# Kernel optimization log

Measured on AMD Instinct MI355X. Metric: run time of the kernel, lower is better.

## Reference

```python
import jax, jax.numpy as jnp
import numpy as np

N, C, F, E = 32768, 256, 1024, 16
TOP_K = 2


def setup_inputs() -> dict:
    key = jax.random.key(0)
    k_x, k_gw, k_w1, k_w2 = jax.random.split(key, 4)
    x = jax.random.normal(k_x, (N, C), dtype=jnp.float32)
    gate_W = jax.random.normal(k_gw, (E, C), dtype=jnp.float32) * 0.01  # nn.init.normal_(std=0.01)
    gate_b = jnp.zeros((E,), dtype=jnp.float32)
    W1 = jax.random.normal(k_w1, (E, C, F), dtype=jnp.float32) * 0.02
    b1 = jnp.zeros((E, F), dtype=jnp.float32)
    W2 = jax.random.normal(k_w2, (E, F, C), dtype=jnp.float32) * 0.02
    b2 = jnp.zeros((E, C), dtype=jnp.float32)
    return {"x": x, "gate_W": gate_W, "gate_b": gate_b,
            "W1": W1, "b1": b1, "W2": W2, "b2": b2}


def reference(x, gate_W, gate_b, W1, b1, W2, b2):
    # Gating (eval mode: no gaussian noise)
    gate_logits = x @ gate_W.T + gate_b                       # [N, E]
    gate_probs = jax.nn.softmax(gate_logits, axis=-1)
    gate_entropy = -(gate_probs * jnp.log(gate_probs + 1e-8)).sum(axis=-1).mean()

    topk_val, topk_idx = jax.lax.top_k(gate_logits, TOP_K)   # [N, K]
    gate_weights = jax.nn.softmax(topk_val, axis=-1)          # softmax over the top-k logits

    # Dense all-expert FFN compute (matches the torch stack over experts)
    h = jax.nn.relu(jnp.einsum('nc,ecf->enf', x, W1) + b1[:, None, :])   # [E, N, F]
    expert_outputs = jnp.einsum('enf,efc->enc', h, W2) + b2[:, None, :]  # [E, N, C]

    # Gather top-k expert outputs per token and combine
    eo = jnp.transpose(expert_outputs, (1, 0, 2))             # [N, E, C]
    selected = jnp.take_along_axis(eo, topk_idx[:, :, None], axis=1)  # [N, K, C]
    out = (gate_weights[:, :, None] * selected).sum(axis=1)  # [N, C]

    # default args: return_gate=False, return_entropy=True
    return out, gate_entropy
```

## Files before the change

kernel.cpp:

```cpp
#include <hip/hip_runtime.h>
#include <hip/hip_bf16.h>
#include <math.h>

#define N_TOK 32768
#define C_DIM 256
#define F_DIM 1024
#define E_NUM 16
#define TILE_R 128
#define NCH 16
#define NBLK 544

typedef unsigned short u16;
typedef unsigned int u32;
typedef __attribute__((ext_vector_type(4))) u16 u16x4;
typedef __attribute__((ext_vector_type(8))) u16 u16x8;
typedef __attribute__((ext_vector_type(8))) short bf16x8;
typedef __attribute__((ext_vector_type(4))) u32 u32x4;
typedef __attribute__((ext_vector_type(16))) float f32x16;

#define AS1 __attribute__((address_space(1)))
#define AS3 __attribute__((address_space(3)))

__device__ __forceinline__ void gload16(const void* g, void* lds) {
    __builtin_amdgcn_global_load_lds((const AS1 u32*)(uintptr_t)g,
                                     (AS3 u32*)(u32)(uintptr_t)lds, 16, 0, 0);
}

__device__ __forceinline__ u16 f2bf(float f) {
    union { float f; u32 u; } v; v.f = f;
    u32 r = v.u + 0x7fffu + ((v.u >> 16) & 1u);
    return (u16)(r >> 16);
}

__device__ __forceinline__ float bf2f(u16 b) {
    union { u32 u; float f; } v; v.u = ((u32)b) << 16;
    return v.f;
}


__global__ __launch_bounds__(256) void gate_kernel(
    const float* __restrict__ x, const float* __restrict__ gW,
    const float* __restrict__ gb, float* __restrict__ ent_out,
    int* __restrict__ tidx, float* __restrict__ tw, int* __restrict__ counts,
    u16* __restrict__ xb)
{
    __shared__ float gws[E_NUM * C_DIM];
    __shared__ float gbs[E_NUM];
    __shared__ float went[4];
    __shared__ int lc[E_NUM];
    int tid = threadIdx.x;

    for (int i = tid; i < E_NUM * C_DIM / 4; i += 256)
        ((float4*)gws)[i] = ((const float4*)gW)[i];
    if (tid < E_NUM) { gbs[tid] = gb[tid]; lc[tid] = 0; }
    __syncthreads();

    int tok = tid >> 2, q = tid & 3;
    int n = blockIdx.x * 64 + tok;
    const float* xr = x + (size_t)n * C_DIM;

    float4 xv[16];
    #pragma unroll
    for (int j = 0; j < 16; j++)
        xv[j] = *(const float4*)(xr + j * 16 + q * 4);

    #pragma unroll
    for (int j = 0; j < 16; j++) {
        u16x4 o;
        o[0] = f2bf(xv[j].x); o[1] = f2bf(xv[j].y);
        o[2] = f2bf(xv[j].z); o[3] = f2bf(xv[j].w);
        *(u16x4*)(xb + (size_t)n * C_DIM + j * 16 + q * 4) = o;
    }

    float lg[E_NUM];
    #pragma unroll
    for (int e = 0; e < E_NUM; e++) lg[e] = 0.f;
    #pragma unroll
    for (int j = 0; j < 16; j++) {
        #pragma unroll
        for (int e = 0; e < E_NUM; e++) {
            float4 g = *(const float4*)(gws + e * C_DIM + j * 16 + q * 4);
            lg[e] += xv[j].x * g.x + xv[j].y * g.y + xv[j].z * g.z + xv[j].w * g.w;
        }
    }
    #pragma unroll
    for (int e = 0; e < E_NUM; e++) {
        lg[e] += __shfl_xor(lg[e], 1);
        lg[e] += __shfl_xor(lg[e], 2);
        lg[e] += gbs[e];
    }

    float m = lg[0];
    #pragma unroll
    for (int e = 1; e < E_NUM; e++) m = fmaxf(m, lg[e]);
    float s = 0.f, ex[E_NUM];
    #pragma unroll
    for (int e = 0; e < E_NUM; e++) { ex[e] = __expf(lg[e] - m); s += ex[e]; }
    float inv = 1.f / s;
    float ent = 0.f;
    #pragma unroll
    for (int e = 0; e < E_NUM; e++) {
        float p = ex[e] * inv;
        ent -= p * logf(p + 1e-8f);
    }

    float v0 = -1e30f, v1 = -1e30f;
    int i0 = 0, i1 = 0;
    #pragma unroll
    for (int e = 0; e < E_NUM; e++) {
        float l = lg[e];
        if (l > v0) { v1 = v0; i1 = i0; v0 = l; i0 = e; }
        else if (l > v1) { v1 = l; i1 = e; }
    }
    if (q == 0) {
        float w1e = __expf(v1 - v0);
        float z = 1.f + w1e;
        tidx[2 * n] = i0; tidx[2 * n + 1] = i1;
        tw[2 * n] = 1.f / z; tw[2 * n + 1] = w1e / z;
        atomicAdd(&lc[i0], 1);
        atomicAdd(&lc[i1], 1);
    }

    float v = ent;
    for (int off = 32; off > 0; off >>= 1) v += __shfl_down(v, off);
    int wid = tid >> 6, lane = tid & 63;
    if (lane == 0) went[wid] = v;
    __syncthreads();
    if (tid == 0)
        atomicAdd(ent_out, (went[0] + went[1] + went[2] + went[3]) * (1.0f / (4.0f * N_TOK)));
    if (tid < E_NUM && lc[tid]) atomicAdd(&counts[tid], lc[tid]);
}

__global__ void prefix_kernel(const int* __restrict__ counts,
                              int* __restrict__ offs, int* __restrict__ tp)
{
    if (threadIdx.x == 0 && blockIdx.x == 0) {
        int o = 0, t = 0;
        offs[0] = 0; tp[0] = 0;
        for (int e = 0; e < E_NUM; e++) {
            o += counts[e];
            t += (counts[e] + TILE_R - 1) / TILE_R;
            offs[e + 1] = o;
            tp[e + 1] = t;
        }
    }
}

__global__ __launch_bounds__(256) void scatter_kernel(
    const int* __restrict__ tidx, const float* __restrict__ tw,
    const int* __restrict__ offs, int* __restrict__ fill,
    int* __restrict__ tok, float* __restrict__ wgt, int* __restrict__ pairpos)
{
    __shared__ int lc[E_NUM], lbase[E_NUM];
    int tid = threadIdx.x;
    if (tid < E_NUM) lc[tid] = 0;
    __syncthreads();
    int n = blockIdx.x * 256 + tid;
    int e0 = tidx[2 * n], e1 = tidx[2 * n + 1];
    int r0 = atomicAdd(&lc[e0], 1);
    int r1 = atomicAdd(&lc[e1], 1);
    __syncthreads();
    if (tid < E_NUM) lbase[tid] = offs[tid] + atomicAdd(&fill[tid], lc[tid]);
    __syncthreads();
    int p0 = lbase[e0] + r0, p1 = lbase[e1] + r1;
    tok[p0] = n; wgt[p0] = tw[2 * n];     pairpos[2 * n] = p0;
    tok[p1] = n; wgt[p1] = tw[2 * n + 1]; pairpos[2 * n + 1] = p1;
}

__global__ __launch_bounds__(256) void tcvt_w1f(
    const float* __restrict__ W1, u16* __restrict__ w1f)
{
    __shared__ float t[256][33];
    int e = blockIdx.x, ft = blockIdx.y;
    int tid = threadIdx.x;
    const float* src = W1 + ((size_t)e * C_DIM) * F_DIM + (size_t)tid * F_DIM + ft * 32;
    #pragma unroll
    for (int j = 0; j < 8; j++) {
        float4 v = *(const float4*)(src + j * 4);
        t[tid][j * 4] = v.x; t[tid][j * 4 + 1] = v.y;
        t[tid][j * 4 + 2] = v.z; t[tid][j * 4 + 3] = v.w;
    }
    __syncthreads();
    int l = tid & 63, ksq = tid >> 6;
    #pragma unroll
    for (int p = 0; p < 4; p++) {
        int ks = ksq * 4 + p;
        int c0 = ks * 16 + (l >> 5) * 8;
        u16x8 o;
        #pragma unroll
        for (int j = 0; j < 8; j++) o[j] = f2bf(t[c0 + j][l & 31]);
        *(u16x8*)(w1f + ((size_t)((e * 32 + ft) * 16 + ks)) * 512 + l * 8) = o;
    }
}

__global__ __launch_bounds__(256) void tcvt_w2f(
    const float* __restrict__ W2, u16* __restrict__ w2f)
{
    __shared__ float t[256][33];
    int e = blockIdx.x, ct = blockIdx.y, fq = blockIdx.z;
    int tid = threadIdx.x;
    const float* src = W2 + ((size_t)e * F_DIM + fq * 256 + tid) * C_DIM + ct * 32;
    #pragma unroll
    for (int j = 0; j < 8; j++) {
        float4 v = *(const float4*)(src + j * 4);
        t[tid][j * 4] = v.x; t[tid][j * 4 + 1] = v.y;
        t[tid][j * 4 + 2] = v.z; t[tid][j * 4 + 3] = v.w;
    }
    __syncthreads();
    int l = tid & 63, kq = tid >> 6;
    #pragma unroll
    for (int p = 0; p < 4; p++) {
        int kfl = kq * 4 + p;
        int f0 = kfl * 16 + (l >> 5) * 8;
        u16x8 o;
        #pragma unroll
        for (int j = 0; j < 8; j++) o[j] = f2bf(t[f0 + j][l & 31]);
        *(u16x8*)(w2f + ((size_t)((e * 8 + ct) * 64 + fq * 16 + kfl)) * 512 + l * 8) = o;
    }
}

#define HS_OFF  135168
#define B1S_OFF 131072

#define STAGE_CHUNK(CHN, NBUF)                                                \
    if (wid < 4) {                                                            \
        _Pragma("unroll")                                                     \
        for (int i = 0; i < 8; i++) {                                         \
            int fid = (wid << 3) + i;                                         \
            gload16(w1fe + (((size_t)((CHN) << 5) + fid) << 9) + (lane << 3), \
                    (NBUF) + (fid << 10));                                    \
        }                                                                     \
    } else {                                                                  \
        _Pragma("unroll")                                                     \
        for (int i = 0; i < 8; i++) {                                         \
            int g = ((wid - 4) << 3) + i;                                     \
            int ct = g >> 2, kfl = g & 3;                                     \
            gload16(w2fe + (((size_t)(ct << 6) + ((CHN) << 2) + kfl) << 9) + (lane << 3), \
                    (NBUF) + 32768 + (g << 10));                              \
        }                                                                     \
    }

template <int MODE>
__global__ __launch_bounds__(512, 2) void ffn_mfma(
    const u16* __restrict__ xb, const u16* __restrict__ w1f,
    const u16* __restrict__ w2f, const float* __restrict__ b1,
    const float* __restrict__ b2, const int* __restrict__ tok,
    const float* __restrict__ wgt, const int* __restrict__ offs,
    const int* __restrict__ tp, u16* __restrict__ ybuf,
    float* __restrict__ out)
{
    __shared__ __align__(1024) char smem[152576];
    int* s_tok = (int*)(smem + 151552);
    float* s_w = (float*)(smem + 152064);
    float* b1s = (float*)(smem + B1S_OFF);

    int bidx = blockIdx.x;
    int b = (bidx & 7) * (NBLK / 8) + (bidx >> 3);
    if (b >= tp[E_NUM]) return;
    int e = 0;
    while (b >= tp[e + 1]) e++;
    int base = offs[e] + ((b - tp[e]) << 7);
    int rows = offs[e + 1] - base; if (rows > TILE_R) rows = TILE_R;

    int tid = threadIdx.x;
    int lane = tid & 63, wid = tid >> 6;
    int hi = lane >> 5;
    int wr = wid >> 1, wc = wid & 1;

    const u16* w1fe = w1f + ((size_t)e << 9) * 512;
    const u16* w2fe = w2f + ((size_t)e << 9) * 512;
    const float* b1e = b1 + e * F_DIM;
    const float* b2e = b2 + e * C_DIM;

    if (tid < TILE_R) {
        int src = (tid < rows) ? base + tid : base;
        s_tok[tid] = tok[src];
        s_w[tid] = (tid < rows) ? wgt[src] : 0.f;
    }
    if (tid < 256) ((float4*)b1s)[tid] = ((const float4*)b1e)[tid];
    __syncthreads();

    #pragma unroll
    for (int i = 0; i < 8; i++) {
        int idx2 = (wid << 3) + i;
        int row = ((idx2 >> 4) << 5) + (lane & 31);
        gload16(xb + ((size_t)s_tok[row] << 8) + ((idx2 & 15) << 4) + (hi << 3),
                smem + (idx2 << 10));
    }
    asm volatile("s_waitcnt vmcnt(0)" ::: "memory");
    __syncthreads();

    bf16x8 xr[16];
    #pragma unroll
    for (int ks = 0; ks < 16; ks++)
        xr[ks] = *(const bf16x8*)(smem + (wr << 14) + (ks << 10) + (lane << 4));
    __syncthreads();

    STAGE_CHUNK(0, smem)
    asm volatile("s_waitcnt vmcnt(0)" ::: "memory");
    __syncthreads();

    f32x16 acc2[4];
    #pragma unroll
    for (int ct = 0; ct < 4; ct++) acc2[ct] = (f32x16)(0.0f);

    for (int ch = 0; ch < NCH; ch++) {
        int cur = ch & 1;
        const char* cbuf = smem + (cur << 16);

        if (ch + 1 < NCH) {
            char* nbuf = smem + ((cur ^ 1) << 16);
            STAGE_CHUNK(ch + 1, nbuf)
        }

        const char* w1b = cbuf + (wc << 14) + (lane << 4);
        f32x16 acc1a = (f32x16)(0.0f), acc1b = (f32x16)(0.0f);
        #pragma unroll
        for (int ks = 0; ks < 8; ks++) {
            bf16x8 a0 = *(const bf16x8*)(w1b + ((2 * ks) << 10));
            bf16x8 a1 = *(const bf16x8*)(w1b + ((2 * ks + 1) << 10));
            acc1a = __builtin_amdgcn_mfma_f32_32x32x16_bf16(a0, xr[2 * ks], acc1a, 0, 0, 0);
            acc1b = __builtin_amdgcn_mfma_f32_32x32x16_bf16(a1, xr[2 * ks + 1], acc1b, 0, 0, 0);
        }

        float h[16];
        #pragma unroll
        for (int r = 0; r < 16; r++) {
            int fl = (wc << 5) + (r & 3) + ((r >> 2) << 3) + (hi << 2);
            h[r] = fmaxf(acc1a[r] + acc1b[r] + b1s[(ch << 6) + fl], 0.f);
        }
        u32 w[8];
        #pragma unroll
        for (int t = 0; t < 8; t++)
            asm("v_cvt_pk_bf16_f32 %0, %1, %2" : "=v"(w[t]) : "v"(h[2 * t]), "v"(h[2 * t + 1]));
        asm volatile("v_permlane32_swap_b32 %0, %1" : "+v"(w[0]), "+v"(w[2]));
        asm volatile("v_permlane32_swap_b32 %0, %1" : "+v"(w[1]), "+v"(w[3]));
        asm volatile("v_permlane32_swap_b32 %0, %1" : "+v"(w[4]), "+v"(w[6]));
        asm volatile("v_permlane32_swap_b32 %0, %1" : "+v"(w[5]), "+v"(w[7]));
        union { u32x4 u; bf16x8 v; } fr0, fr1, pr0, pr1;
        fr0.u = (u32x4){w[0], w[1], w[2], w[3]};
        fr1.u = (u32x4){w[4], w[5], w[6], w[7]};

        *(u32x4*)(smem + HS_OFF + (wr << 12) + ((wc << 1) << 10) + (lane << 4)) = fr0.u;
        *(u32x4*)(smem + HS_OFF + (wr << 12) + (((wc << 1) + 1) << 10) + (lane << 4)) = fr1.u;

        asm volatile("s_waitcnt lgkmcnt(0)" ::: "memory");
        __builtin_amdgcn_s_barrier();
        __builtin_amdgcn_sched_barrier(0);

        pr0.u = *(const u32x4*)(smem + HS_OFF + (wr << 12) + (((wc ^ 1) << 1) << 10) + (lane << 4));
        pr1.u = *(const u32x4*)(smem + HS_OFF + (wr << 12) + ((((wc ^ 1) << 1) + 1) << 10) + (lane << 4));

        const char* w2b = cbuf + 32768 + (wc << 14) + (lane << 4);
        bf16x8 bh0, bh1, bh2, bh3;
        if (wc == 0) { bh0 = fr0.v; bh1 = fr1.v; bh2 = pr0.v; bh3 = pr1.v; }
        else         { bh0 = pr0.v; bh1 = pr1.v; bh2 = fr0.v; bh3 = fr1.v; }

        #define P2_STEP(BH, S2)                                               \
            _Pragma("unroll")                                                 \
            for (int ctl = 0; ctl < 4; ctl++) {                               \
                bf16x8 a = *(const bf16x8*)(w2b + (ctl << 12) + ((S2) << 10));\
                acc2[ctl] = __builtin_amdgcn_mfma_f32_32x32x16_bf16(a, BH, acc2[ctl], 0, 0, 0); \
            }
        P2_STEP(bh0, 0)
        P2_STEP(bh1, 1)
        P2_STEP(bh2, 2)
        P2_STEP(bh3, 3)
        #undef P2_STEP

        asm volatile("s_waitcnt vmcnt(0) lgkmcnt(0)" ::: "memory");
        __builtin_amdgcn_s_barrier();
        __builtin_amdgcn_sched_barrier(0);
    }

    int m = (wr << 5) + (lane & 31);
    if (m < rows) {
        if (MODE == 0) {
            u16* yr = ybuf + ((size_t)(base + m) << 8) + (wc << 7);
            #pragma unroll
            for (int ctl = 0; ctl < 4; ctl++) {
                #pragma unroll
                for (int rq = 0; rq < 4; rq++) {
                    int c = (ctl << 5) + (rq << 3) + (hi << 2);
                    u16x4 o;
                    o[0] = f2bf(acc2[ctl][4 * rq]);
                    o[1] = f2bf(acc2[ctl][4 * rq + 1]);
                    o[2] = f2bf(acc2[ctl][4 * rq + 2]);
                    o[3] = f2bf(acc2[ctl][4 * rq + 3]);
                    *(u16x4*)(yr + c) = o;
                }
            }
        } else {
            float wgt_m = s_w[m];
            float* orow = out + ((size_t)s_tok[m] << 8) + (wc << 7);
            const float* b2w = b2e + (wc << 7);
            #pragma unroll
            for (int ctl = 0; ctl < 4; ctl++) {
                #pragma unroll
                for (int rq = 0; rq < 4; rq++) {
                    int c = (ctl << 5) + (rq << 3) + (hi << 2);
                    #pragma unroll
                    for (int l2 = 0; l2 < 4; l2++)
                        atomicAdd(&orow[c + l2],
                                  wgt_m * (acc2[ctl][4 * rq + l2] + b2w[c + l2]));
                }
            }
        }
    }
}

__global__ __launch_bounds__(256) void combine_kernel(
    const u16* __restrict__ ybuf, const int* __restrict__ tidx,
    const float* __restrict__ tw, const int* __restrict__ pairpos,
    const float* __restrict__ b2, float* __restrict__ out)
{
    int idx = blockIdx.x * 256 + threadIdx.x;
    int n = idx >> 6;
    int q = (idx & 63) << 2;
    int e0 = tidx[2 * n], e1 = tidx[2 * n + 1];
    float w0 = tw[2 * n], w1 = tw[2 * n + 1];
    int p0 = pairpos[2 * n], p1 = pairpos[2 * n + 1];
    u16x4 y0 = *(const u16x4*)(ybuf + ((size_t)p0 << 8) + q);
    u16x4 y1 = *(const u16x4*)(ybuf + ((size_t)p1 << 8) + q);
    float4 c0 = *(const float4*)(b2 + (e0 << 8) + q);
    float4 c1 = *(const float4*)(b2 + (e1 << 8) + q);
    float4 o;
    o.x = w0 * (bf2f(y0[0]) + c0.x) + w1 * (bf2f(y1[0]) + c1.x);
    o.y = w0 * (bf2f(y0[1]) + c0.y) + w1 * (bf2f(y1[1]) + c1.y);
    o.z = w0 * (bf2f(y0[2]) + c0.z) + w1 * (bf2f(y1[2]) + c1.z);
    o.w = w0 * (bf2f(y0[3]) + c0.w) + w1 * (bf2f(y1[3]) + c1.w);
    *(float4*)(out + ((size_t)n << 8) + q) = o;
}

extern "C" void kernel_launch(void* const* d_in, const int* in_sizes, int n_in,
                              void* d_out, int out_size, void* d_ws, size_t ws_size,
                              hipStream_t stream)
{
    const float* x   = (const float*)d_in[0];
    const float* gW  = (const float*)d_in[1];
    const float* gb  = (const float*)d_in[2];
    const float* W1  = (const float*)d_in[3];
    const float* b1  = (const float*)d_in[4];
    const float* W2  = (const float*)d_in[5];
    const float* b2  = (const float*)d_in[6];
    float* out = (float*)d_out;

    char* ws = (char*)d_ws;
    int*   topk_idx = (int*)(ws + 0);
    float* topk_w   = (float*)(ws + 262144);
    int*   tok      = (int*)(ws + 524288);
    float* wgt      = (float*)(ws + 786432);
    int*   pairpos  = (int*)(ws + 1048576);
    int*   counts   = (int*)(ws + 1310720);
    int*   fill     = (int*)(ws + 1310784);
    int*   offs     = (int*)(ws + 1310848);
    int*   tp       = (int*)(ws + 1310916);

    const size_t XB_OFF  = 2097152;
    const size_t W1F_OFF = 18874368;
    const size_t W2F_OFF = 27262976;
    const size_t Y_OFF   = 35651584;
    const size_t WS_FULL = Y_OFF + (size_t)2 * N_TOK * C_DIM * 2;

    u16* xb  = (u16*)(ws + XB_OFF);
    u16* w1f = (u16*)(ws + W1F_OFF);
    u16* w2f = (u16*)(ws + W2F_OFF);
    u16* ybuf = (u16*)(ws + Y_OFF);

    int mode = (ws_size >= WS_FULL) ? 0 : 1;

    float* ent_out = out + (size_t)N_TOK * C_DIM;

    if (mode == 0) {
        hipMemsetAsync(ent_out, 0, sizeof(float), stream);
    } else {
        hipMemsetAsync(d_out, 0, (size_t)(N_TOK * C_DIM + 1) * sizeof(float), stream);
    }
    hipMemsetAsync(counts, 0, 2 * E_NUM * sizeof(int), stream);

    gate_kernel<<<N_TOK / 64, 256, 0, stream>>>(x, gW, gb, ent_out,
                                                topk_idx, topk_w, counts, xb);
    prefix_kernel<<<1, 64, 0, stream>>>(counts, offs, tp);
    scatter_kernel<<<N_TOK / 256, 256, 0, stream>>>(topk_idx, topk_w, offs,
                                                    fill, tok, wgt, pairpos);
    tcvt_w1f<<<dim3(E_NUM, 32), 256, 0, stream>>>(W1, w1f);
    tcvt_w2f<<<dim3(E_NUM, 8, 4), 256, 0, stream>>>(W2, w2f);

    if (mode == 0) {
        ffn_mfma<0><<<NBLK, 512, 0, stream>>>(xb, w1f, w2f, b1, b2, tok, wgt,
                                              offs, tp, ybuf, out);
        combine_kernel<<<N_TOK * 64 / 256, 256, 0, stream>>>(ybuf, topk_idx,
                                                             topk_w, pairpos, b2, out);
    } else {
        ffn_mfma<1><<<NBLK, 512, 0, stream>>>(xb, w1f, w2f, b1, b2, tok, wgt,
                                              offs, tp, ybuf, out);
    }
}
```

Before: 183.5 us.

## Restructure FFN block to 4 waves with full-width rows, dropping h LDS exchange

The expert FFN kernel now uses 256 threads (4 waves). Each wave owns 32 token rows across all 256 output columns instead of splitting columns between wave pairs. F is processed in 32 chunks of 32 rather than 16 chunks of 64. Because each wave has the full hidden slice for its rows, the LDS write/barrier/read exchange of the relu activations between partner waves is removed, and LDS use drops from about 149KB to about 69KB. The cost is twice as many chunk iterations and barriers, twice the acc2 accumulator registers per thread, and fewer waves per block to hide latency.

New measurement: 181.7 us, median of 2. No clear change (-1.0%).

```diff
diff --git a/kernel.cpp b/kernel.cpp
--- a/kernel.cpp
+++ b/kernel.cpp
@@ -7,7 +7,7 @@
 #define F_DIM 1024
 #define E_NUM 16
 #define TILE_R 128
-#define NCH 16
+#define NCH 32
 #define NBLK 544
 
 typedef unsigned short u16;
@@ -219,29 +219,27 @@
     }
 }
 
-#define HS_OFF  135168
-#define B1S_OFF 131072
+#define B1S_OFF 65536
 
 #define STAGE_CHUNK(CHN, NBUF)                                                \
-    if (wid < 4) {                                                            \
+    {                                                                         \
         _Pragma("unroll")                                                     \
-        for (int i = 0; i < 8; i++) {                                         \
-            int fid = (wid << 3) + i;                                         \
-            gload16(w1fe + (((size_t)((CHN) << 5) + fid) << 9) + (lane << 3), \
-                    (NBUF) + (fid << 10));                                    \
+        for (int i = 0; i < 4; i++) {                                         \
+            int ks = (wid << 2) + i;                                          \
+            gload16(w1fe + (((size_t)((CHN) << 4) + ks) << 9) + (lane << 3),  \
+                    (NBUF) + (ks << 10));                                     \
         }                                                                     \
-    } else {                                                                  \
         _Pragma("unroll")                                                     \
-        for (int i = 0; i < 8; i++) {                                         \
-            int g = ((wid - 4) << 3) + i;                                     \
-            int ct = g >> 2, kfl = g & 3;                                     \
-            gload16(w2fe + (((size_t)(ct << 6) + ((CHN) << 2) + kfl) << 9) + (lane << 3), \
-                    (NBUF) + 32768 + (g << 10));                              \
+        for (int i = 0; i < 4; i++) {                                         \
+            int g = (wid << 2) + i;                                           \
+            int ct = g >> 1, s2 = g & 1;                                      \
+            gload16(w2fe + (((size_t)(ct << 6) + ((CHN) << 1) + s2) << 9) + (lane << 3), \
+                    (NBUF) + 16384 + (g << 10));                              \
         }                                                                     \
     }
 
 template <int MODE>
-__global__ __launch_bounds__(512, 2) void ffn_mfma(
+__global__ __launch_bounds__(256, 2) void ffn_mfma(
     const u16* __restrict__ xb, const u16* __restrict__ w1f,
     const u16* __restrict__ w2f, const float* __restrict__ b1,
     const float* __restrict__ b2, const int* __restrict__ tok,
@@ -249,9 +247,9 @@
     const int* __restrict__ tp, u16* __restrict__ ybuf,
     float* __restrict__ out)
 {
-    __shared__ __align__(1024) char smem[152576];
-    int* s_tok = (int*)(smem + 151552);
-    float* s_w = (float*)(smem + 152064);
+    __shared__ __align__(1024) char smem[70656];
+    int* s_tok = (int*)(smem + 69632);
+    float* s_w = (float*)(smem + 70144);
     float* b1s = (float*)(smem + B1S_OFF);
 
     int bidx = blockIdx.x;
@@ -265,7 +263,6 @@
     int tid = threadIdx.x;
     int lane = tid & 63, wid = tid >> 6;
     int hi = lane >> 5;
-    int wr = wid >> 1, wc = wid & 1;
 
     const u16* w1fe = w1f + ((size_t)e << 9) * 512;
     const u16* w2fe = w2f + ((size_t)e << 9) * 512;
@@ -277,12 +274,12 @@
         s_tok[tid] = tok[src];
         s_w[tid] = (tid < rows) ? wgt[src] : 0.f;
     }
-    if (tid < 256) ((float4*)b1s)[tid] = ((const float4*)b1e)[tid];
-    __syncthreads();
-
-    #pragma unroll
-    for (int i = 0; i < 8; i++) {
-        int idx2 = (wid << 3) + i;
+    ((float4*)b1s)[tid] = ((const float4*)b1e)[tid];
+    __syncthreads();
+
+    #pragma unroll
+    for (int i = 0; i < 16; i++) {
+        int idx2 = (wid << 4) + i;
         int row = ((idx2 >> 4) << 5) + (lane & 31);
         gload16(xb + ((size_t)s_tok[row] << 8) + ((idx2 & 15) << 4) + (hi << 3),
                 smem + (idx2 << 10));
@@ -293,27 +290,27 @@
     bf16x8 xr[16];
     #pragma unroll
     for (int ks = 0; ks < 16; ks++)
-        xr[ks] = *(const bf16x8*)(smem + (wr << 14) + (ks << 10) + (lane << 4));
+        xr[ks] = *(const bf16x8*)(smem + (wid << 14) + (ks << 10) + (lane << 4));
     __syncthreads();
 
     STAGE_CHUNK(0, smem)
     asm volatile("s_waitcnt vmcnt(0)" ::: "memory");
     __syncthreads();
 
-    f32x16 acc2[4];
-    #pragma unroll
-    for (int ct = 0; ct < 4; ct++) acc2[ct] = (f32x16)(0.0f);
+    f32x16 acc2[8];
+    #pragma unroll
+    for (int ct = 0; ct < 8; ct++) acc2[ct] = (f32x16)(0.0f);
 
     for (int ch = 0; ch < NCH; ch++) {
         int cur = ch & 1;
-        const char* cbuf = smem + (cur << 16);
+        const char* cbuf = smem + (cur << 15);
 
         if (ch + 1 < NCH) {
-            char* nbuf = smem + ((cur ^ 1) << 16);
+            char* nbuf = smem + ((cur ^ 1) << 15);
             STAGE_CHUNK(ch + 1, nbuf)
         }
 
-        const char* w1b = cbuf + (wc << 14) + (lane << 4);
+        const char* w1b = cbuf + (lane << 4);
         f32x16 acc1a = (f32x16)(0.0f), acc1b = (f32x16)(0.0f);
         #pragma unroll
         for (int ks = 0; ks < 8; ks++) {
@@ -326,8 +323,8 @@
         float h[16];
         #pragma unroll
         for (int r = 0; r < 16; r++) {
-            int fl = (wc << 5) + (r & 3) + ((r >> 2) << 3) + (hi << 2);
-            h[r] = fmaxf(acc1a[r] + acc1b[r] + b1s[(ch << 6) + fl], 0.f);
+            int fl = (r & 3) + ((r >> 2) << 3) + (hi << 2);
+            h[r] = fmaxf(acc1a[r] + acc1b[r] + b1s[(ch << 5) + fl], 0.f);
         }
         u32 w[8];
         #pragma unroll
@@ -337,48 +334,30 @@
         asm volatile("v_permlane32_swap_b32 %0, %1" : "+v"(w[1]), "+v"(w[3]));
         asm volatile("v_permlane32_swap_b32 %0, %1" : "+v"(w[4]), "+v"(w[6]));
         asm volatile("v_permlane32_swap_b32 %0, %1" : "+v"(w[5]), "+v"(w[7]));
-        union { u32x4 u; bf16x8 v; } fr0, fr1, pr0, pr1;
+        union { u32x4 u; bf16x8 v; } fr0, fr1;
         fr0.u = (u32x4){w[0], w[1], w[2], w[3]};
         fr1.u = (u32x4){w[4], w[5], w[6], w[7]};
 
-        *(u32x4*)(smem + HS_OFF + (wr << 12) + ((wc << 1) << 10) + (lane << 4)) = fr0.u;
-        *(u32x4*)(smem + HS_OFF + (wr << 12) + (((wc << 1) + 1) << 10) + (lane << 4)) = fr1.u;
-
-        asm volatile("s_waitcnt lgkmcnt(0)" ::: "memory");
-        __builtin_amdgcn_s_barrier();
-        __builtin_amdgcn_sched_barrier(0);
-
-        pr0.u = *(const u32x4*)(smem + HS_OFF + (wr << 12) + (((wc ^ 1) << 1) << 10) + (lane << 4));
-        pr1.u = *(const u32x4*)(smem + HS_OFF + (wr << 12) + ((((wc ^ 1) << 1) + 1) << 10) + (lane << 4));
-
-        const char* w2b = cbuf + 32768 + (wc << 14) + (lane << 4);
-        bf16x8 bh0, bh1, bh2, bh3;
-        if (wc == 0) { bh0 = fr0.v; bh1 = fr1.v; bh2 = pr0.v; bh3 = pr1.v; }
-        else         { bh0 = pr0.v; bh1 = pr1.v; bh2 = fr0.v; bh3 = fr1.v; }
-
-        #define P2_STEP(BH, S2)                                               \
-            _Pragma("unroll")                                                 \
-            for (int ctl = 0; ctl < 4; ctl++) {                               \
-                bf16x8 a = *(const bf16x8*)(w2b + (ctl << 12) + ((S2) << 10));\
-                acc2[ctl] = __builtin_amdgcn_mfma_f32_32x32x16_bf16(a, BH, acc2[ctl], 0, 0, 0); \
-            }
-        P2_STEP(bh0, 0)
-        P2_STEP(bh1, 1)
-        P2_STEP(bh2, 2)
-        P2_STEP(bh3, 3)
-        #undef P2_STEP
+        const char* w2b = cbuf + 16384 + (lane << 4);
+        #pragma unroll
+        for (int ctl = 0; ctl < 8; ctl++) {
+            bf16x8 a0 = *(const bf16x8*)(w2b + ((ctl << 1) << 10));
+            bf16x8 a1 = *(const bf16x8*)(w2b + (((ctl << 1) + 1) << 10));
+            acc2[ctl] = __builtin_amdgcn_mfma_f32_32x32x16_bf16(a0, fr0.v, acc2[ctl], 0, 0, 0);
+            acc2[ctl] = __builtin_amdgcn_mfma_f32_32x32x16_bf16(a1, fr1.v, acc2[ctl], 0, 0, 0);
+        }
 
         asm volatile("s_waitcnt vmcnt(0) lgkmcnt(0)" ::: "memory");
         __builtin_amdgcn_s_barrier();
         __builtin_amdgcn_sched_barrier(0);
     }
 
-    int m = (wr << 5) + (lane & 31);
+    int m = (wid << 5) + (lane & 31);
     if (m < rows) {
         if (MODE == 0) {
-            u16* yr = ybuf + ((size_t)(base + m) << 8) + (wc << 7);
+            u16* yr = ybuf + ((size_t)(base + m) << 8);
             #pragma unroll
-            for (int ctl = 0; ctl < 4; ctl++) {
+            for (int ctl = 0; ctl < 8; ctl++) {
                 #pragma unroll
                 for (int rq = 0; rq < 4; rq++) {
                     int c = (ctl << 5) + (rq << 3) + (hi << 2);
@@ -392,17 +371,16 @@
             }
         } else {
             float wgt_m = s_w[m];
-            float* orow = out + ((size_t)s_tok[m] << 8) + (wc << 7);
-            const float* b2w = b2e + (wc << 7);
+            float* orow = out + ((size_t)s_tok[m] << 8);
             #pragma unroll
-            for (int ctl = 0; ctl < 4; ctl++) {
+            for (int ctl = 0; ctl < 8; ctl++) {
                 #pragma unroll
                 for (int rq = 0; rq < 4; rq++) {
                     int c = (ctl << 5) + (rq << 3) + (hi << 2);
                     #pragma unroll
                     for (int l2 = 0; l2 < 4; l2++)
                         atomicAdd(&orow[c + l2],
-                                  wgt_m * (acc2[ctl][4 * rq + l2] + b2w[c + l2]));
+                                  wgt_m * (acc2[ctl][4 * rq + l2] + b2e[c + l2]));
                 }
             }
         }
@@ -487,12 +465,12 @@
     tcvt_w2f<<<dim3(E_NUM, 8, 4), 256, 0, stream>>>(W2, w2f);
 
     if (mode == 0) {
-        ffn_mfma<0><<<NBLK, 512, 0, stream>>>(xb, w1f, w2f, b1, b2, tok, wgt,
+        ffn_mfma<0><<<NBLK, 256, 0, stream>>>(xb, w1f, w2f, b1, b2, tok, wgt,
                                               offs, tp, ybuf, out);
         combine_kernel<<<N_TOK * 64 / 256, 256, 0, stream>>>(ybuf, topk_idx,
                                                              topk_w, pairpos, b2, out);
     } else {
-        ffn_mfma<1><<<NBLK, 512, 0, stream>>>(xb, w1f, w2f, b1, b2, tok, wgt,
+        ffn_mfma<1><<<NBLK, 256, 0, stream>>>(xb, w1f, w2f, b1, b2, tok, wgt,
                                               offs, tp, ybuf, out);
     }
 }
```
